# Performance work log

Measured on AMD Instinct MI355X. Metric: run time of the kernel, lower is better.

## Reference

```python
import jax, jax.numpy as jnp
import numpy as np

B, W, K = 16, 128, 128          # batch, window_size, n_features
KS = 7                          # conv kernel size
HG = 256                        # gru_hid_dim
HF = 256                        # forecast_hid_dim
HR = 256                        # recon_hid_dim
OUT = 128                       # out_dim
ALPHA = 0.2                     # leaky relu slope
ED = 2 * W                      # gatv2 embed dims (2*window == 2*features here == 256)


def setup_inputs() -> dict:
    key = jax.random.key(0)
    ks = jax.random.split(key, 32)
    s = lambda k, shp, sc=0.05: (jax.random.normal(k, shp, dtype=jnp.float32) * sc)
    return {
        "x": jax.random.normal(ks[0], (B, W, K), dtype=jnp.float32),
        # ConvLayer
        "conv_w": s(ks[1], (K, K, KS)),
        "conv_b": s(ks[2], (K,)),
        # FeatureAttentionLayer (gatv2): lin 2W->2W, a (2W,1), bias (K,K)
        "fg_lin_w": s(ks[3], (ED, 2 * W)),
        "fg_lin_b": s(ks[4], (ED,)),
        "fg_a": s(ks[5], (ED, 1)),
        "fg_bias": s(ks[6], (K, K)),
        # TemporalAttentionLayer (gatv2): lin 2K->2K, a (2K,1), bias (W,W)
        "tg_lin_w": s(ks[7], (2 * K, 2 * K)),
        "tg_lin_b": s(ks[8], (2 * K,)),
        "tg_a": s(ks[9], (2 * K, 1)),
        "tg_bias": s(ks[10], (W, W)),
        # GRU encoder: input 3K -> HG (torch gate order r,z,n)
        "gru_w_ih": s(ks[11], (3 * HG, 3 * K)),
        "gru_w_hh": s(ks[12], (3 * HG, HG)),
        "gru_b_ih": s(ks[13], (3 * HG,)),
        "gru_b_hh": s(ks[14], (3 * HG,)),
        # Forecasting_Model (n_layers=1 -> two Linears)
        "fc1_w": s(ks[15], (HF, HG)),
        "fc1_b": s(ks[16], (HF,)),
        "fc2_w": s(ks[17], (OUT, HF)),
        "fc2_b": s(ks[18], (OUT,)),
        # ReconstructionModel: decoder GRU HG -> HR, fc HR -> OUT
        "dec_w_ih": s(ks[19], (3 * HR, HG)),
        "dec_w_hh": s(ks[20], (3 * HR, HR)),
        "dec_b_ih": s(ks[21], (3 * HR,)),
        "dec_b_hh": s(ks[22], (3 * HR,)),
        "rec_fc_w": s(ks[23], (OUT, HR)),
        "rec_fc_b": s(ks[24], (OUT,)),
    }


def _gru(x_seq, w_ih, w_hh, b_ih, b_hh):
    """torch-convention GRU over (b, t, d). Returns (outs (b,t,H), h_T (b,H))."""
    H = w_hh.shape[1]
    def step(h, xt):
        gi = xt @ w_ih.T + b_ih
        gh = h @ w_hh.T + b_hh
        ir, iz, inn = jnp.split(gi, 3, axis=-1)
        hr, hz, hn = jnp.split(gh, 3, axis=-1)
        r = jax.nn.sigmoid(ir + hr)
        z = jax.nn.sigmoid(iz + hz)
        n = jnp.tanh(inn + r * hn)
        h_new = (1.0 - z) * n + z * h
        return h_new, h_new
    h0 = jnp.zeros((x_seq.shape[0], H), x_seq.dtype)
    hT, outs = jax.lax.scan(step, h0, jnp.swapaxes(x_seq, 0, 1))
    return jnp.swapaxes(outs, 0, 1), hT


def _gatv2(v, lin_w, lin_b, a, bias):
    """v: (b, N, D). Pairwise concat GATv2 attention, returns sigmoid(attn @ v)."""
    b, N, D = v.shape
    vi = jnp.broadcast_to(v[:, :, None, :], (b, N, N, D))   # node i repeated
    vj = jnp.broadcast_to(v[:, None, :, :], (b, N, N, D))   # node j alternating
    cat = jnp.concatenate([vi, vj], axis=-1)                 # (b, N, N, 2D)
    h = jax.nn.leaky_relu(cat @ lin_w.T + lin_b, ALPHA)      # (b, N, N, ED)
    e = jnp.squeeze(h @ a, -1) + bias                        # (b, N, N)
    attn = jax.nn.softmax(e, axis=2)
    return jax.nn.sigmoid(jnp.einsum('bij,bjd->bid', attn, v))


def reference(x, conv_w, conv_b, fg_lin_w, fg_lin_b, fg_a, fg_bias,
              tg_lin_w, tg_lin_b, tg_a, tg_bias,
              gru_w_ih, gru_w_hh, gru_b_ih, gru_b_hh,
              fc1_w, fc1_b, fc2_w, fc2_b,
              dec_w_ih, dec_w_hh, dec_b_ih, dec_b_hh, rec_fc_w, rec_fc_b):
    # ConvLayer: permute -> pad -> conv1d -> relu -> permute
    xc = jnp.transpose(x, (0, 2, 1))                        # (b, K, W)
    xc = jnp.pad(xc, ((0, 0), (0, 0), ((KS - 1) // 2, (KS - 1) // 2)))
    y = jax.lax.conv_general_dilated(xc, conv_w, (1,), 'VALID',
                                     dimension_numbers=('NCH', 'OIH', 'NCH'))
    xconv = jnp.transpose(jax.nn.relu(y + conv_b[None, :, None]), (0, 2, 1))  # (b, W, K)

    # Feature GAT operates on (b, K, W); output permuted back to (b, W, K)
    h_feat = jnp.transpose(
        _gatv2(jnp.transpose(xconv, (0, 2, 1)), fg_lin_w, fg_lin_b, fg_a, fg_bias),
        (0, 2, 1))
    # Temporal GAT operates on (b, W, K)
    h_temp = _gatv2(xconv, tg_lin_w, tg_lin_b, tg_a, tg_bias)

    h_cat = jnp.concatenate([xconv, h_feat, h_temp], axis=2)  # (b, W, 3K)
    _, h_end = _gru(h_cat, gru_w_ih, gru_w_hh, gru_b_ih, gru_b_hh)  # (b, HG)

    # Forecasting MLP (dropout is identity in eval)
    pred = jax.nn.relu(h_end @ fc1_w.T + fc1_b) @ fc2_w.T + fc2_b   # (b, OUT)

    # ReconstructionModel: repeat_interleave along dim=1 then view (b, W, HG)
    h_rep = jnp.repeat(h_end, W, axis=1).reshape(h_end.shape[0], W, -1)
    dec_out, _ = _gru(h_rep, dec_w_ih, dec_w_hh, dec_b_ih, dec_b_hh)  # (b, W, HR)
    recons = dec_out @ rec_fc_w.T + rec_fc_b                          # (b, W, OUT)

    return pred, recons
```

## Files before the change

### kernel.cpp

```cpp
#include <hip/hip_runtime.h>

typedef _Float16 f16;
typedef _Float16 f16x2 __attribute__((ext_vector_type(2)));
typedef _Float16 f16x4 __attribute__((ext_vector_type(4)));
typedef _Float16 f16x8 __attribute__((ext_vector_type(8)));
typedef float f32x4 __attribute__((ext_vector_type(4)));
typedef unsigned int ui4 __attribute__((ext_vector_type(4)));

__device__ __forceinline__ float fast_rcp(float x) {
#if __has_builtin(__builtin_amdgcn_rcpf)
    return __builtin_amdgcn_rcpf(x);
#else
    return 1.0f / x;
#endif
}
__device__ __forceinline__ float sigmoidf(float x) { return fast_rcp(1.0f + __expf(-x)); }
__device__ __forceinline__ float tanh_f(float x)   { return 2.0f * fast_rcp(1.0f + __expf(-2.0f * x)) - 1.0f; }

__device__ __forceinline__ unsigned int pk2(float a, float b) {
    union { _Float16 h[2]; unsigned int u; } t;
    t.h[0] = (_Float16)a; t.h[1] = (_Float16)b;
    return t.u;
}
__device__ __forceinline__ unsigned short f16bits(float f) {
// ... 10 lines not shown
}
__device__ __forceinline__ float quad_reduce(float x) {
#if __has_builtin(__builtin_amdgcn_mov_dpp)
    int a = __builtin_amdgcn_mov_dpp(__builtin_bit_cast(int, x), 0xB1, 0xF, 0xF, true);
    x += __builtin_bit_cast(float, a);
    int b = __builtin_amdgcn_mov_dpp(__builtin_bit_cast(int, x), 0x4E, 0xF, 0xF, true);
    x += __builtin_bit_cast(float, b);
    return x;
#else
    x += __shfl_xor(x, 1);
    x += __shfl_xor(x, 2);
    return x;
#endif
}


__global__ void prep_kernel(const float* __restrict__ conv_w,
                            const float* __restrict__ fg_lin_w,
                            const float* __restrict__ tg_lin_w,
                            const float* __restrict__ w_ih,
                            const float* __restrict__ w_hh,
                            const float* __restrict__ dec_w_ih,
                            const float* __restrict__ dec_w_hh,
                            const float* __restrict__ rec_fc_w,
                            f16* __restrict__ w_ihB,
                            unsigned int* __restrict__ wpkE,
                            unsigned int* __restrict__ wpkD,
                            float* __restrict__ c01,
                            float* __restrict__ linTf, float* __restrict__ linTt,
                            float* __restrict__ recT, float* __restrict__ convT)
{
    const int blk = blockIdx.x, lane = threadIdx.x;
    const int quad = lane >> 4, lq = lane & 15;
    if (blk < 576) {
        int tau = blk / 12, kk = blk % 12;
        int g = tau % 3, jt = tau / 3;
        int n = g * 256 + jt * 16 + lq;
        int k0 = kk * 32 + quad * 8;
        f16x8 v;
#pragma unroll
        for (int e = 0; e < 8; ++e) v[e] = (f16)w_ih[n * 384 + k0 + e];
        *(f16x8*)&w_ihB[(blk * 64 + lane) * 8] = v;
    } else if (blk < 960) {
        int i2 = blk - 576;
        const float* src = w_hh; unsigned int* dst = wpkE;
        if (i2 >= 192) { i2 -= 192; src = dec_w_hh; dst = wpkD; }
        int r = i2 >> 5, i = i2 & 31;
#pragma unroll
        for (int c = 0; c < 8; ++c) {
            int tidx = lane * 8 + c;
            int jt = tidx >> 2, q = tidx & 3;
            int n = (r >> 1) * 256 + (r & 1) * 128 + jt;
            int k = q * 64 + 2 * i;
            dst[(r * 32 + i) * 512 + tidx] = pk2(src[n * 256 + k], src[n * 256 + k + 1]);
        }
    } else if (blk < 972) {
        int n = (blk - 960) * 64 + lane;
        float s0 = 0.f, s1 = 0.f;
        const float* row = dec_w_ih + (long)n * 256;
        for (int d = 0; d < 128; ++d) { s0 += row[d]; s1 += row[128 + d]; }
        c01[n] = s0; c01[768 + n] = s1;
    } else if (blk < 1484) {
        int i = blk - 972; int mat = i >> 8, d = i & 255;
        const float* src = mat ? tg_lin_w : fg_lin_w;
        float* dst = mat ? linTt : linTf;
#pragma unroll
        for (int c = 0; c < 4; ++c) { int n = lane + 64 * c; dst[d * 256 + n] = src[n * 256 + d]; }
    } else if (blk < 1740) {
        int d = blk - 1484;
#pragma unroll
        for (int c = 0; c < 2; ++c) { int j2 = lane + 64 * c; recT[d * 128 + j2] = rec_fc_w[j2 * 256 + d]; }
    } else {
        int i = blk - 1740;
#pragma unroll
        for (int c = 0; c < 2; ++c) { int co = lane + 64 * c; convT[i * 128 + co] = conv_w[co * 896 + i]; }
    }
}

__global__ void conv_kernel(const float* __restrict__ x,
                            const float* __restrict__ convT,
                            const float* __restrict__ cb,
                            float* __restrict__ h_catT,
                            float* __restrict__ xconvT)
{
    const int wc = blockIdx.x, b = blockIdx.y, tid = threadIdx.x;
    __shared__ float xs[14][128];
    const int w0 = wc * 8;
#pragma unroll
    for (int i = 0; i < 14; ++i) {
        int row = w0 - 3 + i;
        xs[i][tid] = (row >= 0 && row < 128) ? x[(b * 128 + row) * 128 + tid] : 0.f;
    }
    __syncthreads();
    float bias = cb[tid];
    float acc[8];
#pragma unroll
    for (int j = 0; j < 8; ++j) acc[j] = bias;
    for (int ci = 0; ci < 128; ++ci) {
        float wv[7];
#pragma unroll
        for (int t = 0; t < 7; ++t) wv[t] = convT[(ci * 7 + t) * 128 + tid];
#pragma unroll
        for (int t = 0; t < 7; ++t) {
#pragma unroll
            for (int j = 0; j < 8; ++j) acc[j] += xs[j + t][ci] * wv[t];
        }
    }
#pragma unroll
    for (int j = 0; j < 8; ++j) {
        float v = fmaxf(acc[j], 0.f);
        h_catT[((w0 + j) * 16 + b) * 384 + tid] = v;
        xconvT[(b * 128 + tid) * 128 + w0 + j] = v;
    }
}

__global__ void lin_kernel(const float* __restrict__ vsrc, int mode,
                           const float* __restrict__ T,
                           const float* __restrict__ lb,
                           float* __restrict__ P, float* __restrict__ Q)
{
    const int tid = threadIdx.x;
    const int row0 = blockIdx.x * 8;
    __shared__ __align__(16) float vs[8][128];
    if (mode == 0) {
        ((float4*)vs)[tid] = ((const float4*)(vsrc + row0 * 128))[tid];
    } else {
        int b = row0 >> 7;
        int rr = tid >> 5, q = tid & 31;
        int t = (row0 & 127) + rr;
        *(float4*)&vs[rr][q * 4] = *(const float4*)&vsrc[(t * 16 + b) * 384 + q * 4];
    }
    __syncthreads();
    const int n = tid;
    float bias = lb[n];
    float accP[8], accQ[8];
#pragma unroll
    for (int rr = 0; rr < 8; ++rr) { accP[rr] = bias; accQ[rr] = 0.f; }
    for (int d4 = 0; d4 < 32; ++d4) {
        float4 vv[8];
#pragma unroll
        for (int rr = 0; rr < 8; ++rr) vv[rr] = *(const float4*)&vs[rr][d4 * 4];
#pragma unroll
        for (int e = 0; e < 4; ++e) {
            float wP = T[(d4 * 4 + e) * 256 + n];
            float wQ = T[(128 + d4 * 4 + e) * 256 + n];
#pragma unroll
            for (int rr = 0; rr < 8; ++rr) {
                float h = (e == 0) ? vv[rr].x : (e == 1) ? vv[rr].y : (e == 2) ? vv[rr].z : vv[rr].w;
                accP[rr] += h * wP;
                accQ[rr] += h * wQ;
            }
        }
    }
#pragma unroll
    for (int rr = 0; rr < 8; ++rr) {
        P[(long)(row0 + rr) * 256 + n] = accP[rr];
        Q[(long)(row0 + rr) * 256 + n] = accQ[rr];
    }
}

__global__ void gat_kernel(const float* __restrict__ P, const float* __restrict__ Q,
                           const float* __restrict__ a,
                           const float* __restrict__ bias,
                           const float* __restrict__ vbase,
                           float* __restrict__ h_catT, int mode)
{
    const int bid = blockIdx.x;
    const int b = bid >> 7, i = bid & 127;
    const int tid = threadIdx.x;
    __shared__ __align__(16) float Ps[256], as_[256], ej[128], red[8], op[256];
    __shared__ __align__(16) float buf[16384];

    Ps[tid]  = P[(long)(b * 128 + i) * 256 + tid];
    as_[tid] = a[tid];

    const int jl = tid >> 3, c = tid & 7;
    for (int j0 = 0; j0 < 128; j0 += 32) {
        __syncthreads();
#pragma unroll
        for (int r = 0; r < 8; ++r) {
            int flat = r * 256 + tid;
            int jj = flat >> 6, e4 = flat & 63;
            *(float4*)&buf[jj * 264 + e4 * 4] =
                *(const float4*)&Q[(long)(b * 128 + j0 + jj) * 256 + e4 * 4];
        }
        __syncthreads();
        float p = 0.f;
        for (int k = 0; k < 32; ++k) {
            int e = c + 8 * k;
            float hv = Ps[e] + buf[jl * 264 + e];
            hv = (hv > 0.f) ? hv : 0.2f * hv;
            p += hv * as_[e];
        }
        p += __shfl_xor(p, 1);
        p += __shfl_xor(p, 2);
        p += __shfl_xor(p, 4);
        if (c == 0) ej[j0 + jl] = p + bias[i * 128 + j0 + jl];
    }
    __syncthreads();
    {
        float v = (tid < 128) ? ej[tid] : -1e30f;
#pragma unroll
        for (int off = 32; off >= 1; off >>= 1) v = fmaxf(v, __shfl_xor(v, off));
        if ((tid & 63) == 0) red[tid >> 6] = v;
        __syncthreads();
        float m = fmaxf(fmaxf(red[0], red[1]), fmaxf(red[2], red[3]));
        float p = (tid < 128) ? __expf(ej[tid] - m) : 0.f;
        float s = p;
#pragma unroll
        for (int off = 32; off >= 1; off >>= 1) s += __shfl_xor(s, off);
        if ((tid & 63) == 0) red[4 + (tid >> 6)] = s;
        __syncthreads();
        float rs = fast_rcp(red[4] + red[5] + red[6] + red[7]);
        if (tid < 128) ej[tid] = p * rs;
        __syncthreads();
    }
    if (mode == 0) {
        const float4* s = (const float4*)(vbase + (long)b * 16384);
#pragma unroll
        for (int i2 = 0; i2 < 16; ++i2) ((float4*)buf)[i2 * 256 + tid] = s[i2 * 256 + tid];
    } else {
        int row = tid >> 1, hf = tid & 1;
#pragma unroll
        for (int i2 = 0; i2 < 16; ++i2) {
            int cc = (hf * 16 + i2) * 4;
            *(float4*)&buf[row * 128 + cc] = *(const float4*)&vbase[(row * 16 + b) * 384 + cc];
        }
    }
    __syncthreads();
    const int half = tid >> 7, d = tid & 127;
    float p0 = 0.f, p1 = 0.f, p2 = 0.f, p3 = 0.f;
#pragma unroll 4
    for (int j = 0; j < 64; j += 4) {
        int jb = half * 64 + j;
        p0 += ej[jb]     * buf[(jb)     * 128 + d];
        p1 += ej[jb + 1] * buf[(jb + 1) * 128 + d];
        p2 += ej[jb + 2] * buf[(jb + 2) * 128 + d];
        p3 += ej[jb + 3] * buf[(jb + 3) * 128 + d];
    }
    op[tid] = (p0 + p1) + (p2 + p3);
    __syncthreads();
    if (tid < 128) {
        float o = sigmoidf(op[tid] + op[tid + 128]);
        if (mode == 0)
            h_catT[(tid * 16 + b) * 384 + 128 + i] = o;
        else
            h_catT[(i * 16 + b) * 384 + 256 + tid] = o;
    }
}

__global__ void __launch_bounds__(256)
gi_gemm32(const float* __restrict__ h_catT, const f16* __restrict__ w_ihB,
          const float* __restrict__ b_ih, float* __restrict__ gi)
{
    const int t = blockIdx.x, tid = threadIdx.x;
    const int w = tid >> 6, lane = tid & 63, quad = lane >> 4, lq = lane & 15;
    __shared__ __align__(16) f16 hA[16][392];
    {
        int rr = tid >> 4, ii = tid & 15;
#pragma unroll
        for (int i2 = 0; i2 < 6; ++i2) {
            int cc = (ii * 6 + i2) * 4;
            float4 v = *(const float4*)&h_catT[(t * 16 + rr) * 384 + cc];
            f16x4 h; h[0] = (f16)v.x; h[1] = (f16)v.y; h[2] = (f16)v.z; h[3] = (f16)v.w;
            *(f16x4*)&hA[rr][cc] = h;
        }
    }
    int nidx[12];
    float biasv[12];
#pragma unroll
    for (int ti = 0; ti < 12; ++ti) {
        int tau = w * 12 + ti, g = tau % 3, jt = tau / 3;
        nidx[ti] = g * 256 + jt * 16 + lq;
        biasv[ti] = b_ih[nidx[ti]];
    }
    f32x4 acc[12] = {};
    __syncthreads();
    for (int kk = 0; kk < 12; ++kk) {
        f16x8 A = *(const f16x8*)&hA[lq][kk * 32 + quad * 8];
#pragma unroll
        for (int ti = 0; ti < 12; ++ti) {
            f16x8 B = *(const f16x8*)&w_ihB[(((w * 12 + ti) * 12 + kk) * 64 + lane) * 8];
            acc[ti] = __builtin_amdgcn_mfma_f32_16x16x32_f16(A, B, acc[ti], 0, 0, 0);
        }
    }
#pragma unroll
    for (int ti = 0; ti < 12; ++ti)
#pragma unroll
        for (int r = 0; r < 4; ++r) {
            int m = quad * 4 + r;
            gi[((long)m * 128 + t) * 768 + nidx[ti]] = acc[ti][r] + biasv[ti];
        }
}

__global__ void __launch_bounds__(512, 2)
gru_enc(const float* __restrict__ gi,
        const unsigned int* __restrict__ wpk,
        const float* __restrict__ b_hh,
        float* __restrict__ h_end)
{
    const int b = blockIdx.x, tid = threadIdx.x;
    const int jt = tid >> 2, q = tid & 3;
    __shared__ __align__(16) unsigned short hpk[2][296];
    __shared__ __align__(16) float gich[32 * 768];

    unsigned int wr[6][32];
    float bh[6];
    int nidx[6];
#pragma unroll
    for (int r = 0; r < 6; ++r) {
        nidx[r] = (r >> 1) * 256 + (r & 1) * 128 + jt;
        bh[r] = b_hh[nidx[r]];
#pragma unroll
        for (int i = 0; i < 32; ++i) wr[r][i] = wpk[(r * 32 + i) * 512 + tid];
    }
    for (int i = tid; i < 2 * 296; i += 512) ((unsigned short*)hpk)[i] = 0;
    float h0 = 0.f, h1 = 0.f;
    const float* gib = gi + (long)b * 128 * 768;

    for (int cchunk = 0; cchunk < 4; ++cchunk) {
        const float* gsrc = gib + (long)cchunk * 32 * 768;
#pragma unroll
        for (int i = 0; i < 12; ++i) {
            int idx = (i * 512 + tid) * 4;
            *(float4*)&gich[idx] = *(const float4*)&gsrc[idx];
        }
        __syncthreads();
        for (int tt = 0; tt < 32; ++tt) {
            const int t = cchunk * 32 + tt;
            const int par = t & 1;
            float gv[6];
#pragma unroll
            for (int r = 0; r < 6; ++r) gv[r] = gich[tt * 768 + nidx[r]];
            float aa[6][2] = {};
            const ui4* hp = (const ui4*)&hpk[par][q * 72];
#pragma unroll
            for (int i = 0; i < 8; ++i) {
                ui4 hv = hp[i];
#pragma unroll
                for (int e = 0; e < 4; ++e) {
#pragma unroll
                    for (int r = 0; r < 6; ++r)
                        aa[r][e & 1] = dot2f(wr[r][i * 4 + e], hv[e], aa[r][e & 1]);
                }
            }
            float s[6];
#pragma unroll
            for (int r = 0; r < 6; ++r) s[r] = quad_reduce(aa[r][0] + aa[r][1]);
            float r0 = sigmoidf(gv[0] + s[0] + bh[0]);
            float r1 = sigmoidf(gv[1] + s[1] + bh[1]);
            float z0 = sigmoidf(gv[2] + s[2] + bh[2]);
            float z1 = sigmoidf(gv[3] + s[3] + bh[3]);
            float n0 = tanh_f(gv[4] + r0 * (s[4] + bh[4]));
            float n1 = tanh_f(gv[5] + r1 * (s[5] + bh[5]));
            h0 = (1.f - z0) * n0 + z0 * h0;
            h1 = (1.f - z1) * n1 + z1 * h1;
            if (q == 0) {
                hpk[par ^ 1][(jt >> 6) * 72 + (jt & 63)]       = f16bits(h0);
                hpk[par ^ 1][(2 + (jt >> 6)) * 72 + (jt & 63)] = f16bits(h1);
            }
            __syncthreads();
        }
    }
    if (q == 0) {
        h_end[b * 256 + jt]       = h0;
        h_end[b * 256 + 128 + jt] = h1;
    }
}

__global__ void __launch_bounds__(512, 2)
gru_dec(const float* __restrict__ h_end,
        const unsigned int* __restrict__ wpk,
        const float* __restrict__ dec_b_hh,
        const float* __restrict__ c01,
        const float* __restrict__ dec_b_ih,
        float* __restrict__ dec_out)
{
    const int b = blockIdx.x, tid = threadIdx.x;
    const int jt = tid >> 2, q = tid & 3;
    __shared__ __align__(16) unsigned short hpk[2][296];
    __shared__ float he[256];
    __shared__ __align__(16) float decbuf[32 * 256];

    unsigned int wr[6][32];
    float bh[6], c0[6], c1[6], bi[6];
    int nidx[6];
#pragma unroll
    for (int r = 0; r < 6; ++r) {
        nidx[r] = (r >> 1) * 256 + (r & 1) * 128 + jt;
        bh[r] = dec_b_hh[nidx[r]];
        bi[r] = dec_b_ih[nidx[r]];
        c0[r] = c01[nidx[r]];
        c1[r] = c01[768 + nidx[r]];
#pragma unroll
        for (int i = 0; i < 32; ++i) wr[r][i] = wpk[(r * 32 + i) * 512 + tid];
    }
    for (int i = tid; i < 2 * 296; i += 512) ((unsigned short*)hpk)[i] = 0;
    if (tid < 256) he[tid] = h_end[b * 256 + tid];
    float h0 = 0.f, h1 = 0.f;
    __syncthreads();

    for (int cchunk = 0; cchunk < 4; ++cchunk) {
        for (int tt = 0; tt < 32; ++tt) {
            const int t = cchunk * 32 + tt;
            const int par = t & 1;
            float e0 = he[2 * t], e1 = he[2 * t + 1];
            float aa[6][2] = {};
            const ui4* hp = (const ui4*)&hpk[par][q * 72];
#pragma unroll
            for (int i = 0; i < 8; ++i) {
                ui4 hv = hp[i];
#pragma unroll
                for (int e = 0; e < 4; ++e) {
#pragma unroll
                    for (int r = 0; r < 6; ++r)
                        aa[r][e & 1] = dot2f(wr[r][i * 4 + e], hv[e], aa[r][e & 1]);
                }
            }
            float s[6], giv[6];
#pragma unroll
            for (int r = 0; r < 6; ++r) {
                s[r] = quad_reduce(aa[r][0] + aa[r][1]);
                giv[r] = e0 * c0[r] + e1 * c1[r] + bi[r];
            }
            float r0 = sigmoidf(giv[0] + s[0] + bh[0]);
            float r1 = sigmoidf(giv[1] + s[1] + bh[1]);
            float z0 = sigmoidf(giv[2] + s[2] + bh[2]);
            float z1 = sigmoidf(giv[3] + s[3] + bh[3]);
            float n0 = tanh_f(giv[4] + r0 * (s[4] + bh[4]));
            float n1 = tanh_f(giv[5] + r1 * (s[5] + bh[5]));
            h0 = (1.f - z0) * n0 + z0 * h0;
            h1 = (1.f - z1) * n1 + z1 * h1;
            if (q == 0) {
                hpk[par ^ 1][(jt >> 6) * 72 + (jt & 63)]       = f16bits(h0);
                hpk[par ^ 1][(2 + (jt >> 6)) * 72 + (jt & 63)] = f16bits(h1);
                decbuf[tt * 256 + jt]       = h0;
                decbuf[tt * 256 + 128 + jt] = h1;
            }
            __syncthreads();
        }
#pragma unroll
        for (int i = 0; i < 4; ++i) {
            int idx = (i * 512 + tid) * 4;
            *(float4*)&dec_out[(long)b * 32768 + cchunk * 8192 + idx] = *(const float4*)&decbuf[idx];
        }
        __syncthreads();
    }
}

__global__ void mlp_kernel(const float* __restrict__ h_end,
                           const float* __restrict__ fc1_w,
                           const float* __restrict__ fc1_b,
                           const float* __restrict__ fc2_w,
                           const float* __restrict__ fc2_b,
                           float* __restrict__ out)
{
    const int b = blockIdx.x, tid = threadIdx.x;
    __shared__ __align__(16) float hv[256], hid[256];
    hv[tid] = h_end[b * 256 + tid];
    __syncthreads();
    float acc = fc1_b[tid], acc2 = 0.f;
    const float4* wr = (const float4*)(fc1_w + tid * 256);
#pragma unroll 4
    for (int i = 0; i < 64; i += 2) {
        float4 w0 = wr[i], w1 = wr[i + 1];
        float4 h0 = *(const float4*)&hv[i * 4], h1 = *(const float4*)&hv[i * 4 + 4];
        acc  += w0.x * h0.x + w0.y * h0.y + w0.z * h0.z + w0.w * h0.w;
        acc2 += w1.x * h1.x + w1.y * h1.y + w1.z * h1.z + w1.w * h1.w;
    }
    hid[tid] = fmaxf(acc + acc2, 0.f);
    __syncthreads();
    if (tid < 128) {
        float a2 = fc2_b[tid], a3 = 0.f;
        const float4* w2 = (const float4*)(fc2_w + tid * 256);
#pragma unroll 4
        for (int i = 0; i < 64; i += 2) {
            float4 w0 = w2[i], w1 = w2[i + 1];
            float4 h0 = *(const float4*)&hid[i * 4], h1 = *(const float4*)&hid[i * 4 + 4];
            a2 += w0.x * h0.x + w0.y * h0.y + w0.z * h0.z + w0.w * h0.w;
            a3 += w1.x * h1.x + w1.y * h1.y + w1.z * h1.z + w1.w * h1.w;
        }
        out[b * 128 + tid] = a2 + a3;
    }
}

__global__ void recon_kernel(const float* __restrict__ dec_out,
                             const float* __restrict__ recT,
                             const float* __restrict__ rec_b,
                             float* __restrict__ out)
{
    const int blk = blockIdx.x, tid = threadIdx.x;
    __shared__ __align__(16) float dv[8][256];
#pragma unroll
    for (int i = 0; i < 2; ++i)
        ((float4*)dv)[i * 256 + tid] = ((const float4*)(dec_out + blk * 2048))[i * 256 + tid];
    __syncthreads();
    const int j = tid & 127, rh = tid >> 7;
// ... 38 lines not shown
    const float* gru_w_hh = (const float*)d_in[12];
    const float* gru_b_ih = (const float*)d_in[13];
    const float* gru_b_hh = (const float*)d_in[14];
    const float* fc1_w    = (const float*)d_in[15];
    const float* fc1_b    = (const float*)d_in[16];
    const float* fc2_w    = (const float*)d_in[17];
    const float* fc2_b    = (const float*)d_in[18];
    const float* dec_w_ih = (const float*)d_in[19];
    const float* dec_w_hh = (const float*)d_in[20];
    const float* dec_b_ih = (const float*)d_in[21];
    const float* dec_b_hh = (const float*)d_in[22];
    const float* rec_fc_w = (const float*)d_in[23];
    const float* rec_fc_b = (const float*)d_in[24];
    float* out = (float*)d_out;

    float* ws      = (float*)d_ws;
    float* h_catT  = ws;
    float* xconvT  = ws + 786432;
    float* Pf      = ws + 1048576;
    float* Qf      = ws + 1572864;
    float* Pt      = ws + 2097152;
    float* Qt      = ws + 2621440;
    float* gi      = Pf;
    f16*   w_ihB   = (f16*)(ws + 3932160);
    unsigned int* wpkE = (unsigned int*)(ws + 4079616);
    unsigned int* wpkD = (unsigned int*)(ws + 4177920);
    float* c01     = ws + 4276224;
    float* linTf   = ws + 4374528;
    float* linTt   = ws + 4440064;
    float* recT    = ws + 4505600;
    float* h_end   = ws + 4538368;
    float* dec_out = ws + 4542464;
    float* convT   = dec_out;

    prep_kernel<<<2636, 64, 0, stream>>>(conv_w, fg_lin_w, tg_lin_w, gru_w_ih, gru_w_hh,
                                         dec_w_ih, dec_w_hh, rec_fc_w,
                                         w_ihB, wpkE, wpkD, c01, linTf, linTt, recT, convT);
    conv_kernel<<<dim3(16, 16), 128, 0, stream>>>(x, convT, conv_b, h_catT, xconvT);
    lin_kernel<<<256, 256, 0, stream>>>(xconvT, 0, linTf, fg_lin_b, Pf, Qf);
    lin_kernel<<<256, 256, 0, stream>>>(h_catT, 1, linTt, tg_lin_b, Pt, Qt);
    gat_kernel<<<2048, 256, 0, stream>>>(Pf, Qf, fg_a, fg_bias, xconvT, h_catT, 0);
    gat_kernel<<<2048, 256, 0, stream>>>(Pt, Qt, tg_a, tg_bias, h_catT, h_catT, 1);
    gi_gemm32<<<128, 256, 0, stream>>>(h_catT, w_ihB, gru_b_ih, gi);
    gru_enc<<<16, 512, 0, stream>>>(gi, wpkE, gru_b_hh, h_end);
    mlp_kernel<<<16, 256, 0, stream>>>(h_end, fc1_w, fc1_b, fc2_w, fc2_b, out);
    gru_dec<<<16, 512, 0, stream>>>(h_end, wpkD, dec_b_hh, c01, dec_b_ih, dec_out);
    recon_kernel<<<256, 256, 0, stream>>>(dec_out, recT, rec_fc_b, out + 2048);
}
```

Baseline: 707.9 us.

## Fuse prep, conv, linear, GAT and gi GEMM into one persistent kernel with grid barriers

Merges the weight prep, convolution, both linear projections, both GAT passes and presumably the input GEMM into one persistent 240-block kernel. The stages are separated by a software grid barrier built on global atomics. The encoder GRU, forecasting MLP and decoder GRU are merged into one kernel, so h_end stays in shared memory. The goal is to remove about ten kernel launches and the gaps between them. In exchange, some stages have fewer blocks or threads per work unit. The spin barrier also assumes all 240 blocks are co-resident on the GPU.

```diff
diff --git a/kernel.cpp b/kernel.cpp
--- a/kernel.cpp
+++ b/kernel.cpp
@@ -48,295 +48,341 @@
 #endif
 }
 
-
-__global__ void prep_kernel(const float* __restrict__ conv_w,
-                            const float* __restrict__ fg_lin_w,
-                            const float* __restrict__ tg_lin_w,
-                            const float* __restrict__ w_ih,
-                            const float* __restrict__ w_hh,
-                            const float* __restrict__ dec_w_ih,
-                            const float* __restrict__ dec_w_hh,
-                            const float* __restrict__ rec_fc_w,
-                            f16* __restrict__ w_ihB,
-                            unsigned int* __restrict__ wpkE,
-                            unsigned int* __restrict__ wpkD,
-                            float* __restrict__ c01,
-                            float* __restrict__ linTf, float* __restrict__ linTt,
-                            float* __restrict__ recT, float* __restrict__ convT)
-{
-    const int blk = blockIdx.x, lane = threadIdx.x;
-    const int quad = lane >> 4, lq = lane & 15;
-    if (blk < 576) {
-        int tau = blk / 12, kk = blk % 12;
-        int g = tau % 3, jt = tau / 3;
-        int n = g * 256 + jt * 16 + lq;
-        int k0 = kk * 32 + quad * 8;
-        f16x8 v;
-#pragma unroll
-        for (int e = 0; e < 8; ++e) v[e] = (f16)w_ih[n * 384 + k0 + e];
-        *(f16x8*)&w_ihB[(blk * 64 + lane) * 8] = v;
-    } else if (blk < 960) {
-        int i2 = blk - 576;
-        const float* src = w_hh; unsigned int* dst = wpkE;
-        if (i2 >= 192) { i2 -= 192; src = dec_w_hh; dst = wpkD; }
-        int r = i2 >> 5, i = i2 & 31;
-#pragma unroll
-        for (int c = 0; c < 8; ++c) {
-            int tidx = lane * 8 + c;
-            int jt = tidx >> 2, q = tidx & 3;
-            int n = (r >> 1) * 256 + (r & 1) * 128 + jt;
-            int k = q * 64 + 2 * i;
-            dst[(r * 32 + i) * 512 + tidx] = pk2(src[n * 256 + k], src[n * 256 + k + 1]);
-        }
-    } else if (blk < 972) {
-        int n = (blk - 960) * 64 + lane;
-        float s0 = 0.f, s1 = 0.f;
-        const float* row = dec_w_ih + (long)n * 256;
-        for (int d = 0; d < 128; ++d) { s0 += row[d]; s1 += row[128 + d]; }
-        c01[n] = s0; c01[768 + n] = s1;
-    } else if (blk < 1484) {
-        int i = blk - 972; int mat = i >> 8, d = i & 255;
-        const float* src = mat ? tg_lin_w : fg_lin_w;
-        float* dst = mat ? linTt : linTf;
-#pragma unroll
-        for (int c = 0; c < 4; ++c) { int n = lane + 64 * c; dst[d * 256 + n] = src[n * 256 + d]; }
-    } else if (blk < 1740) {
-        int d = blk - 1484;
-#pragma unroll
-        for (int c = 0; c < 2; ++c) { int j2 = lane + 64 * c; recT[d * 128 + j2] = rec_fc_w[j2 * 256 + d]; }
-    } else {
-        int i = blk - 1740;
-#pragma unroll
-        for (int c = 0; c < 2; ++c) { int co = lane + 64 * c; convT[i * 128 + co] = conv_w[co * 896 + i]; }
-    }
-}
-
-__global__ void conv_kernel(const float* __restrict__ x,
-                            const float* __restrict__ convT,
-                            const float* __restrict__ cb,
-                            float* __restrict__ h_catT,
-                            float* __restrict__ xconvT)
-{
-    const int wc = blockIdx.x, b = blockIdx.y, tid = threadIdx.x;
-    __shared__ float xs[14][128];
-    const int w0 = wc * 8;
-#pragma unroll
-    for (int i = 0; i < 14; ++i) {
-        int row = w0 - 3 + i;
-        xs[i][tid] = (row >= 0 && row < 128) ? x[(b * 128 + row) * 128 + tid] : 0.f;
-    }
+__device__ __forceinline__ void gbar(unsigned int* bar, int nb) {
     __syncthreads();
-    float bias = cb[tid];
-    float acc[8];
-#pragma unroll
-    for (int j = 0; j < 8; ++j) acc[j] = bias;
-    for (int ci = 0; ci < 128; ++ci) {
-        float wv[7];
-#pragma unroll
-        for (int t = 0; t < 7; ++t) wv[t] = convT[(ci * 7 + t) * 128 + tid];
-#pragma unroll
-        for (int t = 0; t < 7; ++t) {
-#pragma unroll
-            for (int j = 0; j < 8; ++j) acc[j] += xs[j + t][ci] * wv[t];
-        }
-    }
-#pragma unroll
-    for (int j = 0; j < 8; ++j) {
-        float v = fmaxf(acc[j], 0.f);
-        h_catT[((w0 + j) * 16 + b) * 384 + tid] = v;
-        xconvT[(b * 128 + tid) * 128 + w0 + j] = v;
-    }
-}
-
-__global__ void lin_kernel(const float* __restrict__ vsrc, int mode,
-                           const float* __restrict__ T,
-                           const float* __restrict__ lb,
-                           float* __restrict__ P, float* __restrict__ Q)
+    __threadfence();
+    if (threadIdx.x == 0) {
+        unsigned int g = __hip_atomic_load(&bar[1], __ATOMIC_ACQUIRE, __HIP_MEMORY_SCOPE_AGENT);
+        unsigned int old = __hip_atomic_fetch_add(&bar[0], 1u, __ATOMIC_ACQ_REL, __HIP_MEMORY_SCOPE_AGENT);
+        if (old == (unsigned int)nb - 1) {
+            __hip_atomic_store(&bar[0], 0u, __ATOMIC_RELAXED, __HIP_MEMORY_SCOPE_AGENT);
+            __hip_atomic_fetch_add(&bar[1], 1u, __ATOMIC_RELEASE, __HIP_MEMORY_SCOPE_AGENT);
+        } else {
+            while (__hip_atomic_load(&bar[1], __ATOMIC_ACQUIRE, __HIP_MEMORY_SCOPE_AGENT) == g)
+                __builtin_amdgcn_s_sleep(8);
+        }
+    }
+    __syncthreads();
+}
+
+
+__global__ void __launch_bounds__(256)
+fused_feeder(const float* __restrict__ x,
+             const float* __restrict__ conv_w, const float* __restrict__ conv_b,
+             const float* __restrict__ fg_lin_w, const float* __restrict__ fg_lin_b,
+             const float* __restrict__ fg_a, const float* __restrict__ fg_bias,
+             const float* __restrict__ tg_lin_w, const float* __restrict__ tg_lin_b,
+             const float* __restrict__ tg_a, const float* __restrict__ tg_bias,
+             const float* __restrict__ w_ih, const float* __restrict__ w_hh,
+             const float* __restrict__ b_ih,
+             const float* __restrict__ dec_w_ih, const float* __restrict__ dec_w_hh,
+             const float* __restrict__ rec_fc_w,
+             float* __restrict__ ws, unsigned int* __restrict__ bar)
 {
     const int tid = threadIdx.x;
-    const int row0 = blockIdx.x * 8;
-    __shared__ __align__(16) float vs[8][128];
-    if (mode == 0) {
-        ((float4*)vs)[tid] = ((const float4*)(vsrc + row0 * 128))[tid];
-    } else {
-        int b = row0 >> 7;
-        int rr = tid >> 5, q = tid & 31;
-        int t = (row0 & 127) + rr;
-        *(float4*)&vs[rr][q * 4] = *(const float4*)&vsrc[(t * 16 + b) * 384 + q * 4];
-    }
-    __syncthreads();
-    const int n = tid;
-    float bias = lb[n];
-    float accP[8], accQ[8];
-#pragma unroll
-    for (int rr = 0; rr < 8; ++rr) { accP[rr] = bias; accQ[rr] = 0.f; }
-    for (int d4 = 0; d4 < 32; ++d4) {
-        float4 vv[8];
-#pragma unroll
-        for (int rr = 0; rr < 8; ++rr) vv[rr] = *(const float4*)&vs[rr][d4 * 4];
-#pragma unroll
-        for (int e = 0; e < 4; ++e) {
-            float wP = T[(d4 * 4 + e) * 256 + n];
-            float wQ = T[(128 + d4 * 4 + e) * 256 + n];
+    const int nb  = gridDim.x;
+    float* h_catT  = ws;
+    float* xconvT  = ws + 786432;
+    float* Pf      = ws + 1048576;
+    float* Qf      = ws + 1572864;
+    float* Pt      = ws + 2097152;
+    float* Qt      = ws + 2621440;
+    float* gi      = Pf;
+    f16*   w_ihB   = (f16*)(ws + 3932160);
+    unsigned int* wpkE = (unsigned int*)(ws + 4079616);
+    unsigned int* wpkD = (unsigned int*)(ws + 4177920);
+    float* c01     = ws + 4276224;
+    float* linTf   = ws + 4374528;
+    float* linTt   = ws + 4440064;
+    float* recT    = ws + 4505600;
+    float* convT   = ws + 4542464;
+
+    __shared__ __align__(16) char smem[12800];
+
+    {
+        const int warp = tid >> 6, lane = tid & 63;
+        const int quad = lane >> 4, lq = lane & 15;
+        for (int blk = blockIdx.x * 4 + warp; blk < 2636; blk += nb * 4) {
+            if (blk < 576) {
+                int tau = blk / 12, kk = blk % 12;
+                int g = tau % 3, jt = tau / 3;
+                int n = g * 256 + jt * 16 + lq;
+                int k0 = kk * 32 + quad * 8;
+                f16x8 v;
+#pragma unroll
+                for (int e = 0; e < 8; ++e) v[e] = (f16)w_ih[n * 384 + k0 + e];
+                *(f16x8*)&w_ihB[(blk * 64 + lane) * 8] = v;
+            } else if (blk < 960) {
+                int i2 = blk - 576;
+                const float* src = w_hh; unsigned int* dst = wpkE;
+                if (i2 >= 192) { i2 -= 192; src = dec_w_hh; dst = wpkD; }
+                int r = i2 >> 5, i = i2 & 31;
+#pragma unroll
+                for (int c = 0; c < 8; ++c) {
+                    int tidx = lane * 8 + c;
+                    int jt = tidx >> 2, q = tidx & 3;
+                    int n = (r >> 1) * 256 + (r & 1) * 128 + jt;
+                    int k = q * 64 + 2 * i;
+                    dst[(r * 32 + i) * 512 + tidx] = pk2(src[n * 256 + k], src[n * 256 + k + 1]);
+                }
+            } else if (blk < 972) {
+                int n = (blk - 960) * 64 + lane;
+                float s0 = 0.f, s1 = 0.f;
+                const float* row = dec_w_ih + (long)n * 256;
+                for (int d = 0; d < 128; ++d) { s0 += row[d]; s1 += row[128 + d]; }
+                c01[n] = s0; c01[768 + n] = s1;
+            } else if (blk < 1484) {
+                int i = blk - 972; int mat = i >> 8, d = i & 255;
+                const float* src = mat ? tg_lin_w : fg_lin_w;
+                float* dst = mat ? linTt : linTf;
+#pragma unroll
+                for (int c = 0; c < 4; ++c) { int n = lane + 64 * c; dst[d * 256 + n] = src[n * 256 + d]; }
+            } else if (blk < 1740) {
+                int d = blk - 1484;
+#pragma unroll
+                for (int c = 0; c < 2; ++c) { int j2 = lane + 64 * c; recT[d * 128 + j2] = rec_fc_w[j2 * 256 + d]; }
+            } else {
+                int i = blk - 1740;
+#pragma unroll
+                for (int c = 0; c < 2; ++c) { int co = lane + 64 * c; convT[i * 128 + co] = conv_w[co * 896 + i]; }
+            }
+        }
+    }
+    gbar(bar, nb);
+
+    {
+        float (*xs)[128] = (float(*)[128])smem;
+        for (int u = blockIdx.x; u < 256; u += nb) {
+            const int wc = u >> 4, b = u & 15, w0 = wc * 8;
+            for (int i = tid; i < 14 * 128; i += 256) {
+                int r = i >> 7, ci = i & 127;
+                int row = w0 - 3 + r;
+                xs[r][ci] = (row >= 0 && row < 128) ? x[(b * 128 + row) * 128 + ci] : 0.f;
+            }
+            __syncthreads();
+            const int co = tid & 127, jh = tid >> 7;
+            float bias = conv_b[co];
+            float acc[4];
+#pragma unroll
+            for (int j = 0; j < 4; ++j) acc[j] = bias;
+            for (int ci = 0; ci < 128; ++ci) {
+                float wv[7];
+#pragma unroll
+                for (int t = 0; t < 7; ++t) wv[t] = convT[(ci * 7 + t) * 128 + co];
+#pragma unroll
+                for (int t = 0; t < 7; ++t)
+#pragma unroll
+                    for (int j = 0; j < 4; ++j) acc[j] += xs[jh * 4 + j + t][ci] * wv[t];
+            }
+#pragma unroll
+            for (int j = 0; j < 4; ++j) {
+                float v = fmaxf(acc[j], 0.f);
+                int jo = jh * 4 + j;
+                h_catT[((w0 + jo) * 16 + b) * 384 + co] = v;
+                xconvT[(b * 128 + co) * 128 + w0 + jo] = v;
+            }
+            __syncthreads();
+        }
+    }
+    gbar(bar, nb);
+
+    {
+        float (*vs)[128] = (float(*)[128])smem;
+        for (int u = blockIdx.x; u < 512; u += nb) {
+            const int mat = u >> 8;
+            const int row0 = (u & 255) * 8;
+            const float* T  = mat ? linTt : linTf;
+            const float* lb = mat ? tg_lin_b : fg_lin_b;
+            float* P = mat ? Pt : Pf;
+            float* Q = mat ? Qt : Qf;
+            if (mat == 0) {
+                ((float4*)vs)[tid] = ((const float4*)(xconvT + row0 * 128))[tid];
+            } else {
+                int b = row0 >> 7;
+                int rr = tid >> 5, q = tid & 31;
+                int t = (row0 & 127) + rr;
+                *(float4*)&vs[rr][q * 4] = *(const float4*)&h_catT[(t * 16 + b) * 384 + q * 4];
+            }
+            __syncthreads();
+            const int n = tid;
+            float bias = lb[n];
+            float accP[8], accQ[8];
+#pragma unroll
+            for (int rr = 0; rr < 8; ++rr) { accP[rr] = bias; accQ[rr] = 0.f; }
+            for (int d4 = 0; d4 < 32; ++d4) {
+                float4 vv[8];
+#pragma unroll
+                for (int rr = 0; rr < 8; ++rr) vv[rr] = *(const float4*)&vs[rr][d4 * 4];
+#pragma unroll
+                for (int e = 0; e < 4; ++e) {
+                    float wP = T[(d4 * 4 + e) * 256 + n];
+                    float wQ = T[(128 + d4 * 4 + e) * 256 + n];
+#pragma unroll
+                    for (int rr = 0; rr < 8; ++rr) {
+                        float h = (e == 0) ? vv[rr].x : (e == 1) ? vv[rr].y : (e == 2) ? vv[rr].z : vv[rr].w;
+                        accP[rr] += h * wP;
+                        accQ[rr] += h * wQ;
+                    }
+                }
+            }
 #pragma unroll
             for (int rr = 0; rr < 8; ++rr) {
-                float h = (e == 0) ? vv[rr].x : (e == 1) ? vv[rr].y : (e == 2) ? vv[rr].z : vv[rr].w;
-                accP[rr] += h * wP;
-                accQ[rr] += h * wQ;
-            }
-        }
-    }
-#pragma unroll
-    for (int rr = 0; rr < 8; ++rr) {
-        P[(long)(row0 + rr) * 256 + n] = accP[rr];
-        Q[(long)(row0 + rr) * 256 + n] = accQ[rr];
-    }
-}
-
-__global__ void gat_kernel(const float* __restrict__ P, const float* __restrict__ Q,
-                           const float* __restrict__ a,
-                           const float* __restrict__ bias,
-                           const float* __restrict__ vbase,
-                           float* __restrict__ h_catT, int mode)
-{
-    const int bid = blockIdx.x;
-    const int b = bid >> 7, i = bid & 127;
-    const int tid = threadIdx.x;
-    __shared__ __align__(16) float Ps[256], as_[256], ej[128], red[8], op[256];
-    __shared__ __align__(16) float buf[16384];
-
-    Ps[tid]  = P[(long)(b * 128 + i) * 256 + tid];
-    as_[tid] = a[tid];
-
-    const int jl = tid >> 3, c = tid & 7;
-    for (int j0 = 0; j0 < 128; j0 += 32) {
+                P[(long)(row0 + rr) * 256 + n] = accP[rr];
+                Q[(long)(row0 + rr) * 256 + n] = accQ[rr];
+            }
+            __syncthreads();
+        }
+    }
+    gbar(bar, nb);
+
+    {
+        float* ej  = (float*)smem;
+        float* red = ej + 128;
+        float* op  = red + 8;
+        const int c = tid & 7, jl = tid >> 3;
+        for (int u = blockIdx.x; u < 4096; u += nb) {
+            const int mode = u >> 11, b = (u >> 7) & 15, i = u & 127;
+            const float* P_ = mode ? Pt : Pf;
+            const float* Q_ = mode ? Qt : Qf;
+            const float* a_ = mode ? tg_a : fg_a;
+            const float* bias_ = mode ? tg_bias : fg_bias;
+            f32x4 Preg[8], areg[8];
+#pragma unroll
+            for (int k = 0; k < 8; ++k) {
+                Preg[k] = *(const f32x4*)&P_[(long)(b * 128 + i) * 256 + c * 4 + 32 * k];
+                areg[k] = *(const f32x4*)&a_[c * 4 + 32 * k];
+            }
+#pragma unroll
+            for (int jj = 0; jj < 4; ++jj) {
+                const int j = jl + 32 * jj;
+                const float* qrow = &Q_[(long)(b * 128 + j) * 256];
+                float p = 0.f;
+#pragma unroll
+                for (int k = 0; k < 8; ++k) {
+                    f32x4 qv = *(const f32x4*)&qrow[c * 4 + 32 * k];
+#pragma unroll
+                    for (int e = 0; e < 4; ++e) {
+                        float hv = Preg[k][e] + qv[e];
+                        hv = (hv > 0.f) ? hv : 0.2f * hv;
+                        p += hv * areg[k][e];
+                    }
+                }
+                p += __shfl_xor(p, 1);
+                p += __shfl_xor(p, 2);
+                p += __shfl_xor(p, 4);
+                if (c == 0) ej[j] = p + bias_[i * 128 + j];
+            }
+            __syncthreads();
+            {
+                float v = (tid < 128) ? ej[tid] : -1e30f;
+#pragma unroll
+                for (int off = 32; off >= 1; off >>= 1) v = fmaxf(v, __shfl_xor(v, off));
+                if ((tid & 63) == 0) red[tid >> 6] = v;
+                __syncthreads();
+                float m = fmaxf(fmaxf(red[0], red[1]), fmaxf(red[2], red[3]));
+                float p = (tid < 128) ? __expf(ej[tid] - m) : 0.f;
+                float s = p;
+#pragma unroll
+                for (int off = 32; off >= 1; off >>= 1) s += __shfl_xor(s, off);
+                if ((tid & 63) == 0) red[4 + (tid >> 6)] = s;
+                __syncthreads();
+                float rs = fast_rcp(red[4] + red[5] + red[6] + red[7]);
+                if (tid < 128) ej[tid] = p * rs;
+                __syncthreads();
+            }
+            const int half = tid >> 7, d = tid & 127;
+            float p0 = 0.f, p1 = 0.f, p2 = 0.f, p3 = 0.f;
+#pragma unroll 4
+            for (int jx = 0; jx < 64; jx += 4) {
+                int jb = half * 64 + jx;
+                if (mode == 0) {
+                    const float* vb = xconvT + (long)(b * 128 + jb) * 128 + d;
+                    p0 += ej[jb]     * vb[0];
+                    p1 += ej[jb + 1] * vb[128];
+                    p2 += ej[jb + 2] * vb[256];
+                    p3 += ej[jb + 3] * vb[384];
+                } else {
+                    p0 += ej[jb]     * h_catT[((jb)     * 16 + b) * 384 + d];
+                    p1 += ej[jb + 1] * h_catT[((jb + 1) * 16 + b) * 384 + d];
+                    p2 += ej[jb + 2] * h_catT[((jb + 2) * 16 + b) * 384 + d];
+                    p3 += ej[jb + 3] * h_catT[((jb + 3) * 16 + b) * 384 + d];
+                }
+            }
+            op[tid] = (p0 + p1) + (p2 + p3);
+            __syncthreads();
+            if (tid < 128) {
+                float o = sigmoidf(op[tid] + op[tid + 128]);
+                if (mode == 0)
+                    h_catT[(tid * 16 + b) * 384 + 128 + i] = o;
+                else
+                    h_catT[(i * 16 + b) * 384 + 256 + tid] = o;
+            }
+            __syncthreads();
+        }
+    }
+    gbar(bar, nb);
+
+    if (blockIdx.x < 128) {
+        const int t = blockIdx.x;
+        const int w = tid >> 6, lane = tid & 63, quad = lane >> 4, lq = lane & 15;
+        f16 (*hA)[392] = (f16(*)[392])smem;
+        {
+            int rr = tid >> 4, ii = tid & 15;
+#pragma unroll
+            for (int i2 = 0; i2 < 6; ++i2) {
+                int cc = (ii * 6 + i2) * 4;
+                float4 v = *(const float4*)&h_catT[(t * 16 + rr) * 384 + cc];
+                f16x4 h; h[0] = (f16)v.x; h[1] = (f16)v.y; h[2] = (f16)v.z; h[3] = (f16)v.w;
+                *(f16x4*)&hA[rr][cc] = h;
+            }
+        }
+        int nidx[12];
+        float biasv[12];
+#pragma unroll
+        for (int ti = 0; ti < 12; ++ti) {
+            int tau = w * 12 + ti, g = tau % 3, jt = tau / 3;
+            nidx[ti] = g * 256 + jt * 16 + lq;
+            biasv[ti] = b_ih[nidx[ti]];
+        }
+        f32x4 acc[12] = {};
         __syncthreads();
-#pragma unroll
-        for (int r = 0; r < 8; ++r) {
-            int flat = r * 256 + tid;
-            int jj = flat >> 6, e4 = flat & 63;
-            *(float4*)&buf[jj * 264 + e4 * 4] =
-                *(const float4*)&Q[(long)(b * 128 + j0 + jj) * 256 + e4 * 4];
-        }
-        __syncthreads();
-        float p = 0.f;
-        for (int k = 0; k < 32; ++k) {
-            int e = c + 8 * k;
-            float hv = Ps[e] + buf[jl * 264 + e];
-            hv = (hv > 0.f) ? hv : 0.2f * hv;
-            p += hv * as_[e];
-        }
-        p += __shfl_xor(p, 1);
-        p += __shfl_xor(p, 2);
-        p += __shfl_xor(p, 4);
-        if (c == 0) ej[j0 + jl] = p + bias[i * 128 + j0 + jl];
-    }
-    __syncthreads();
-    {
-        float v = (tid < 128) ? ej[tid] : -1e30f;
-#pragma unroll
-        for (int off = 32; off >= 1; off >>= 1) v = fmaxf(v, __shfl_xor(v, off));
-        if ((tid & 63) == 0) red[tid >> 6] = v;
-        __syncthreads();
-        float m = fmaxf(fmaxf(red[0], red[1]), fmaxf(red[2], red[3]));
-        float p = (tid < 128) ? __expf(ej[tid] - m) : 0.f;
-        float s = p;
-#pragma unroll
-        for (int off = 32; off >= 1; off >>= 1) s += __shfl_xor(s, off);
-        if ((tid & 63) == 0) red[4 + (tid >> 6)] = s;
-        __syncthreads();
-        float rs = fast_rcp(red[4] + red[5] + red[6] + red[7]);
-        if (tid < 128) ej[tid] = p * rs;
-        __syncthreads();
-    }
-    if (mode == 0) {
-        const float4* s = (const float4*)(vbase + (long)b * 16384);
-#pragma unroll
-        for (int i2 = 0; i2 < 16; ++i2) ((float4*)buf)[i2 * 256 + tid] = s[i2 * 256 + tid];
-    } else {
-        int row = tid >> 1, hf = tid & 1;
-#pragma unroll
-        for (int i2 = 0; i2 < 16; ++i2) {
-            int cc = (hf * 16 + i2) * 4;
-            *(float4*)&buf[row * 128 + cc] = *(const float4*)&vbase[(row * 16 + b) * 384 + cc];
-        }
-    }
-    __syncthreads();
-    const int half = tid >> 7, d = tid & 127;
-    float p0 = 0.f, p1 = 0.f, p2 = 0.f, p3 = 0.f;
-#pragma unroll 4
-    for (int j = 0; j < 64; j += 4) {
-        int jb = half * 64 + j;
-        p0 += ej[jb]     * buf[(jb)     * 128 + d];
-        p1 += ej[jb + 1] * buf[(jb + 1) * 128 + d];
-        p2 += ej[jb + 2] * buf[(jb + 2) * 128 + d];
-        p3 += ej[jb + 3] * buf[(jb + 3) * 128 + d];
-    }
-    op[tid] = (p0 + p1) + (p2 + p3);
-    __syncthreads();
-    if (tid < 128) {
-        float o = sigmoidf(op[tid] + op[tid + 128]);
-        if (mode == 0)
-            h_catT[(tid * 16 + b) * 384 + 128 + i] = o;
-        else
-            h_catT[(i * 16 + b) * 384 + 256 + tid] = o;
-    }
-}
-
-__global__ void __launch_bounds__(256)
-gi_gemm32(const float* __restrict__ h_catT, const f16* __restrict__ w_ihB,
-          const float* __restrict__ b_ih, float* __restrict__ gi)
-{
-    const int t = blockIdx.x, tid = threadIdx.x;
-    const int w = tid >> 6, lane = tid & 63, quad = lane >> 4, lq = lane & 15;
-    __shared__ __align__(16) f16 hA[16][392];
-    {
-        int rr = tid >> 4, ii = tid & 15;
-#pragma unroll
-        for (int i2 = 0; i2 < 6; ++i2) {
-            int cc = (ii * 6 + i2) * 4;
-            float4 v = *(const float4*)&h_catT[(t * 16 + rr) * 384 + cc];
-            f16x4 h; h[0] = (f16)v.x; h[1] = (f16)v.y; h[2] = (f16)v.z; h[3] = (f16)v.w;
-            *(f16x4*)&hA[rr][cc] = h;
-        }
-    }
-    int nidx[12];
-    float biasv[12];
-#pragma unroll
-    for (int ti = 0; ti < 12; ++ti) {
-        int tau = w * 12 + ti, g = tau % 3, jt = tau / 3;
-        nidx[ti] = g * 256 + jt * 16 + lq;
-        biasv[ti] = b_ih[nidx[ti]];
-    }
-    f32x4 acc[12] = {};
-    __syncthreads();
-    for (int kk = 0; kk < 12; ++kk) {
-        f16x8 A = *(const f16x8*)&hA[lq][kk * 32 + quad * 8];
-#pragma unroll
-        for (int ti = 0; ti < 12; ++ti) {
-            f16x8 B = *(const f16x8*)&w_ihB[(((w * 12 + ti) * 12 + kk) * 64 + lane) * 8];
-            acc[ti] = __builtin_amdgcn_mfma_f32_16x16x32_f16(A, B, acc[ti], 0, 0, 0);
-        }
-    }
-#pragma unroll
-    for (int ti = 0; ti < 12; ++ti)
-#pragma unroll
-        for (int r = 0; r < 4; ++r) {
-            int m = quad * 4 + r;
-            gi[((long)m * 128 + t) * 768 + nidx[ti]] = acc[ti][r] + biasv[ti];
-        }
+        for (int kk = 0; kk < 12; ++kk) {
+            f16x8 A = *(const f16x8*)&hA[lq][kk * 32 + quad * 8];
+#pragma unroll
+            for (int ti = 0; ti < 12; ++ti) {
+                f16x8 B = *(const f16x8*)&w_ihB[(((w * 12 + ti) * 12 + kk) * 64 + lane) * 8];
+                acc[ti] = __builtin_amdgcn_mfma_f32_16x16x32_f16(A, B, acc[ti], 0, 0, 0);
+            }
+        }
+#pragma unroll
+        for (int ti = 0; ti < 12; ++ti)
+#pragma unroll
+            for (int r = 0; r < 4; ++r) {
+                int m = quad * 4 + r;
+                gi[((long)m * 128 + t) * 768 + nidx[ti]] = acc[ti][r] + biasv[ti];
+            }
+    }
 }
 
 __global__ void __launch_bounds__(512, 2)
-gru_enc(const float* __restrict__ gi,
-        const unsigned int* __restrict__ wpk,
+gru_all(const float* __restrict__ gi,
+        const unsigned int* __restrict__ wpkE,
         const float* __restrict__ b_hh,
-        float* __restrict__ h_end)
+        const unsigned int* __restrict__ wpkD,
+        const float* __restrict__ dec_b_hh,
+        const float* __restrict__ c01,
+        const float* __restrict__ dec_b_ih,
+        const float* __restrict__ fc1_w, const float* __restrict__ fc1_b,
+        const float* __restrict__ fc2_w, const float* __restrict__ fc2_b,
+        float* __restrict__ out_pred,
+        float* __restrict__ dec_out)
 {
     const int b = blockIdx.x, tid = threadIdx.x;
     const int jt = tid >> 2, q = tid & 3;
+    __shared__ __align__(16) float gich[32 * 768];
     __shared__ __align__(16) unsigned short hpk[2][296];
-    __shared__ __align__(16) float gich[32 * 768];
+    __shared__ float he[256];
+    __shared__ float hid[256];
 
     unsigned int wr[6][32];
     float bh[6];
@@ -346,7 +392,7 @@
         nidx[r] = (r >> 1) * 256 + (r & 1) * 128 + jt;
         bh[r] = b_hh[nidx[r]];
 #pragma unroll
-        for (int i = 0; i < 32; ++i) wr[r][i] = wpk[(r * 32 + i) * 512 + tid];
+        for (int i = 0; i < 32; ++i) wr[r][i] = wpkE[(r * 32 + i) * 512 + tid];
     }
     for (int i = tid; i < 2 * 296; i += 512) ((unsigned short*)hpk)[i] = 0;
     float h0 = 0.f, h1 = 0.f;
@@ -372,11 +418,10 @@
             for (int i = 0; i < 8; ++i) {
                 ui4 hv = hp[i];
 #pragma unroll
-                for (int e = 0; e < 4; ++e) {
+                for (int e = 0; e < 4; ++e)
 #pragma unroll
                     for (int r = 0; r < 6; ++r)
                         aa[r][e & 1] = dot2f(wr[r][i * 4 + e], hv[e], aa[r][e & 1]);
-                }
             }
             float s[6];
 #pragma unroll
@@ -396,42 +441,55 @@
             __syncthreads();
         }
     }
-    if (q == 0) {
-        h_end[b * 256 + jt]       = h0;
-        h_end[b * 256 + 128 + jt] = h1;
-    }
-}
-
-__global__ void __launch_bounds__(512, 2)
-gru_dec(const float* __restrict__ h_end,
-        const unsigned int* __restrict__ wpk,
-        const float* __restrict__ dec_b_hh,
-        const float* __restrict__ c01,
-        const float* __restrict__ dec_b_ih,
-        float* __restrict__ dec_out)
-{
-    const int b = blockIdx.x, tid = threadIdx.x;
-    const int jt = tid >> 2, q = tid & 3;
-    __shared__ __align__(16) unsigned short hpk[2][296];
-    __shared__ float he[256];
-    __shared__ __align__(16) float decbuf[32 * 256];
-
-    unsigned int wr[6][32];
-    float bh[6], c0[6], c1[6], bi[6];
-    int nidx[6];
+    if (q == 0) { he[jt] = h0; he[128 + jt] = h1; }
+    __syncthreads();
+
+    {
+        const int j = tid >> 1, hf = tid & 1;
+        const float4* wrk = (const float4*)(fc1_w + (long)j * 256 + hf * 128);
+        const float4* hv4 = (const float4*)&he[hf * 128];
+        float a0 = 0.f, a1 = 0.f;
+#pragma unroll 4
+        for (int i = 0; i < 32; i += 2) {
+            float4 w0 = wrk[i], w1 = wrk[i + 1];
+            float4 v0 = hv4[i], v1 = hv4[i + 1];
+            a0 += w0.x * v0.x + w0.y * v0.y + w0.z * v0.z + w0.w * v0.w;
+            a1 += w1.x * v1.x + w1.y * v1.y + w1.z * v1.z + w1.w * v1.w;
+        }
+        float s = a0 + a1;
+        s += __shfl_xor(s, 1);
+        if (!hf) hid[j] = fmaxf(s + fc1_b[j], 0.f);
+    }
+    __syncthreads();
+    {
+        const int j = tid >> 2, q2 = tid & 3;
+        const float4* wrk = (const float4*)(fc2_w + (long)j * 256 + q2 * 64);
+        const float4* hv4 = (const float4*)&hid[q2 * 64];
+        float a0 = 0.f, a1 = 0.f;
+#pragma unroll 4
+        for (int i = 0; i < 16; i += 2) {
+            float4 w0 = wrk[i], w1 = wrk[i + 1];
+            float4 v0 = hv4[i], v1 = hv4[i + 1];
+            a0 += w0.x * v0.x + w0.y * v0.y + w0.z * v0.z + w0.w * v0.w;
+            a1 += w1.x * v1.x + w1.y * v1.y + w1.z * v1.z + w1.w * v1.w;
+        }
+        float s = quad_reduce(a0 + a1);
+        if (q2 == 0) out_pred[b * 128 + j] = s + fc2_b[j];
+    }
+
+    float c0[6], c1[6], bi[6];
 #pragma unroll
     for (int r = 0; r < 6; ++r) {
-        nidx[r] = (r >> 1) * 256 + (r & 1) * 128 + jt;
         bh[r] = dec_b_hh[nidx[r]];
         bi[r] = dec_b_ih[nidx[r]];
         c0[r] = c01[nidx[r]];
         c1[r] = c01[768 + nidx[r]];
 #pragma unroll
-        for (int i = 0; i < 32; ++i) wr[r][i] = wpk[(r * 32 + i) * 512 + tid];
+        for (int i = 0; i < 32; ++i) wr[r][i] = wpkD[(r * 32 + i) * 512 + tid];
     }
     for (int i = tid; i < 2 * 296; i += 512) ((unsigned short*)hpk)[i] = 0;
-    if (tid < 256) he[tid] = h_end[b * 256 + tid];
-    float h0 = 0.f, h1 = 0.f;
+    h0 = 0.f; h1 = 0.f;
+    float* decbuf = gich;
     __syncthreads();
 
     for (int cchunk = 0; cchunk < 4; ++cchunk) {
@@ -445,11 +503,10 @@
             for (int i = 0; i < 8; ++i) {
                 ui4 hv = hp[i];
 #pragma unroll
-                for (int e = 0; e < 4; ++e) {
+                for (int e = 0; e < 4; ++e)
 #pragma unroll
                     for (int r = 0; r < 6; ++r)
                         aa[r][e & 1] = dot2f(wr[r][i * 4 + e], hv[e], aa[r][e & 1]);
-                }
             }
             float s[6], giv[6];
 #pragma unroll
@@ -479,42 +536,6 @@
             *(float4*)&dec_out[(long)b * 32768 + cchunk * 8192 + idx] = *(const float4*)&decbuf[idx];
         }
         __syncthreads();
-    }
-}
-
-__global__ void mlp_kernel(const float* __restrict__ h_end,
-                           const float* __restrict__ fc1_w,
-                           const float* __restrict__ fc1_b,
-                           const float* __restrict__ fc2_w,
-                           const float* __restrict__ fc2_b,
-                           float* __restrict__ out)
-{
-    const int b = blockIdx.x, tid = threadIdx.x;
-    __shared__ __align__(16) float hv[256], hid[256];
-    hv[tid] = h_end[b * 256 + tid];
-    __syncthreads();
-    float acc = fc1_b[tid], acc2 = 0.f;
-    const float4* wr = (const float4*)(fc1_w + tid * 256);
-#pragma unroll 4
-    for (int i = 0; i < 64; i += 2) {
-        float4 w0 = wr[i], w1 = wr[i + 1];
-        float4 h0 = *(const float4*)&hv[i * 4], h1 = *(const float4*)&hv[i * 4 + 4];
-        acc  += w0.x * h0.x + w0.y * h0.y + w0.z * h0.z + w0.w * h0.w;
-        acc2 += w1.x * h1.x + w1.y * h1.y + w1.z * h1.z + w1.w * h1.w;
-    }
-    hid[tid] = fmaxf(acc + acc2, 0.f);
-    __syncthreads();
-    if (tid < 128) {
-        float a2 = fc2_b[tid], a3 = 0.f;
-        const float4* w2 = (const float4*)(fc2_w + tid * 256);
-#pragma unroll 4
-        for (int i = 0; i < 64; i += 2) {
-            float4 w0 = w2[i], w1 = w2[i + 1];
-            float4 h0 = *(const float4*)&hid[i * 4], h1 = *(const float4*)&hid[i * 4 + 4];
-            a2 += w0.x * h0.x + w0.y * h0.y + w0.z * h0.z + w0.w * h0.w;
-            a3 += w1.x * h1.x + w1.y * h1.y + w1.z * h1.z + w1.w * h1.w;
-        }
-        out[b * 128 + tid] = a2 + a3;
     }
 }
 
@@ -583,36 +604,23 @@
     const float* rec_fc_b = (const float*)d_in[24];
     float* out = (float*)d_out;
 
-    float* ws      = (float*)d_ws;
-    float* h_catT  = ws;
-    float* xconvT  = ws + 786432;
-    float* Pf      = ws + 1048576;
-    float* Qf      = ws + 1572864;
-    float* Pt      = ws + 2097152;
-    float* Qt      = ws + 2621440;
-    float* gi      = Pf;
-    f16*   w_ihB   = (f16*)(ws + 3932160);
+    float* ws = (float*)d_ws;
+    float* gi      = ws + 1048576;
     unsigned int* wpkE = (unsigned int*)(ws + 4079616);
     unsigned int* wpkD = (unsigned int*)(ws + 4177920);
     float* c01     = ws + 4276224;
-    float* linTf   = ws + 4374528;
-    float* linTt   = ws + 4440064;
     float* recT    = ws + 4505600;
-    float* h_end   = ws + 4538368;
+    unsigned int* bar = (unsigned int*)(ws + 4538368);
     float* dec_out = ws + 4542464;
-    float* convT   = dec_out;
-
-    prep_kernel<<<2636, 64, 0, stream>>>(conv_w, fg_lin_w, tg_lin_w, gru_w_ih, gru_w_hh,
-                                         dec_w_ih, dec_w_hh, rec_fc_w,
-                                         w_ihB, wpkE, wpkD, c01, linTf, linTt, recT, convT);
-    conv_kernel<<<dim3(16, 16), 128, 0, stream>>>(x, convT, conv_b, h_catT, xconvT);
-    lin_kernel<<<256, 256, 0, stream>>>(xconvT, 0, linTf, fg_lin_b, Pf, Qf);
-    lin_kernel<<<256, 256, 0, stream>>>(h_catT, 1, linTt, tg_lin_b, Pt, Qt);
-    gat_kernel<<<2048, 256, 0, stream>>>(Pf, Qf, fg_a, fg_bias, xconvT, h_catT, 0);
-    gat_kernel<<<2048, 256, 0, stream>>>(Pt, Qt, tg_a, tg_bias, h_catT, h_catT, 1);
-    gi_gemm32<<<128, 256, 0, stream>>>(h_catT, w_ihB, gru_b_ih, gi);
-    gru_enc<<<16, 512, 0, stream>>>(gi, wpkE, gru_b_hh, h_end);
-    mlp_kernel<<<16, 256, 0, stream>>>(h_end, fc1_w, fc1_b, fc2_w, fc2_b, out);
-    gru_dec<<<16, 512, 0, stream>>>(h_end, wpkD, dec_b_hh, c01, dec_b_ih, dec_out);
+
+    hipMemsetAsync(bar, 0, 64, stream);
+    fused_feeder<<<240, 256, 0, stream>>>(x, conv_w, conv_b,
+                                          fg_lin_w, fg_lin_b, fg_a, fg_bias,
+                                          tg_lin_w, tg_lin_b, tg_a, tg_bias,
+                                          gru_w_ih, gru_w_hh, gru_b_ih,
+                                          dec_w_ih, dec_w_hh, rec_fc_w,
+                                          ws, bar);
+    gru_all<<<16, 512, 0, stream>>>(gi, wpkE, gru_b_hh, wpkD, dec_b_hh, c01, dec_b_ih,
+                                    fc1_w, fc1_b, fc2_w, fc2_b, out, dec_out);
     recon_kernel<<<256, 256, 0, stream>>>(dec_out, recT, rec_fc_b, out + 2048);
 }
```

New measurement: 1.324 ms. 1.87x slower.
